# Kernel optimization log

Measured on AMD Instinct MI355X. Metric: run time of the kernel, lower is better.

## Reference

```python
import jax, jax.numpy as jnp
import numpy as np
from jax import lax

B, C, H, W = 32, 256, 64, 64
EPS = 1e-5


def setup_inputs() -> dict:
    key = jax.random.key(0)
    ks = jax.random.split(key, 4)
    x = jax.random.normal(ks[0], (B, C, H, W), dtype=jnp.float32)
    def mk(k):
        kw, = jax.random.split(k, 1)
        w = jax.random.normal(kw, (1, 2, 7, 7), dtype=jnp.float32) * 0.1  # OIHW
        gamma = jnp.ones((1,), jnp.float32)
        beta = jnp.zeros((1,), jnp.float32)
        rmean = jnp.zeros((1,), jnp.float32)
        rvar = jnp.ones((1,), jnp.float32)
        return w, gamma, beta, rmean, rvar
    w1, g1, b1, m1, v1 = mk(ks[1])
    w2, g2, b2, m2, v2 = mk(ks[2])
    w3, g3, b3, m3, v3 = mk(ks[3])
    return dict(x=x,
                w1=w1, g1=g1, b1=b1, m1=m1, v1=v1,
                w2=w2, g2=g2, b2=b2, m2=m2, v2=v2,
                w3=w3, g3=g3, b3=b3, m3=m3, v3=v3)


def _conv_bn_sig(p, w, gamma, beta, mean, var):
    # p: [B,2,h,w]; 7x7 conv 2->1, pad 3, no bias; BN (inference); sigmoid
    y = lax.conv_general_dilated(p, w, window_strides=(1, 1),
                                 padding=[(3, 3), (3, 3)],
                                 dimension_numbers=('NCHW', 'OIHW', 'NCHW'))
    r = lambda t: t.reshape(1, -1, 1, 1)
    y = (y - r(mean)) * (r(gamma) / jnp.sqrt(r(var) + EPS)) + r(beta)
    return jax.nn.sigmoid(y)


def reference(x, w1, g1, b1, m1, v1, w2, g2, b2, m2, v2, w3, g3, b3, m3, v3):
    # In this implementation the permutes cancel: all three branches pool over C.
    mx = jnp.max(x, axis=1, keepdims=True)
    av = jnp.mean(x, axis=1, keepdims=True)
    pooled = jnp.concatenate([mx, av], axis=1)              # [B,2,H,W]
    a1 = _conv_bn_sig(pooled, w1, g1, b1, m1, v1)           # [B,1,H,W]
    p2 = jnp.transpose(pooled, (0, 1, 3, 2))                # [B,2,W,H]
    a2 = jnp.transpose(_conv_bn_sig(p2, w2, g2, b2, m2, v2), (0, 1, 3, 2))
    a3 = _conv_bn_sig(pooled, w3, g3, b3, m3, v3)
    att = (a1 + a2 + a3) / 3.0
    return x * att
```

## Files before the change

### kernel.cpp

```cpp
#include <hip/hip_runtime.h>
#include <math.h>

#define NB 32
#define NC 256
#define NH 64
#define NW 64
#define NHW (NH * NW)
#define EPS_ 1e-5f

typedef float f32x4 __attribute__((ext_vector_type(4)));

__global__ __launch_bounds__(512) void pool_k(const float* __restrict__ x,
                                              float* __restrict__ pooled) {
    const int tid = threadIdx.x;
    const int chunk = tid >> 6;
    const int lane = tid & 63;
    const int q = blockIdx.x * 64 + lane;
    const int b = q >> 10;
    const int hwq = q & 1023;

    const float4* __restrict__ xq = (const float4*)x;
    const int base = b * NC * (NHW / 4) + hwq;

    float4 mx = make_float4(-INFINITY, -INFINITY, -INFINITY, -INFINITY);
    float4 sm = make_float4(0.f, 0.f, 0.f, 0.f);
    const int c0 = chunk * 32;
    #pragma unroll 8
    for (int c = c0; c < c0 + 32; ++c) {
        float4 v = xq[base + c * (NHW / 4)];
        mx.x = fmaxf(mx.x, v.x); mx.y = fmaxf(mx.y, v.y);
        mx.z = fmaxf(mx.z, v.z); mx.w = fmaxf(mx.w, v.w);
        sm.x += v.x; sm.y += v.y; sm.z += v.z; sm.w += v.w;
    }

    __shared__ float4 smax[8][64];
    __shared__ float4 ssum[8][64];
    smax[chunk][lane] = mx;
    ssum[chunk][lane] = sm;
    __syncthreads();

    if (tid < 64) {
        float4 m = smax[0][tid];
        float4 s = ssum[0][tid];
        #pragma unroll
        for (int k = 1; k < 8; ++k) {
            float4 m2 = smax[k][tid];
            float4 s2 = ssum[k][tid];
            m.x = fmaxf(m.x, m2.x); m.y = fmaxf(m.y, m2.y);
            m.z = fmaxf(m.z, m2.z); m.w = fmaxf(m.w, m2.w);
            s.x += s2.x; s.y += s2.y; s.z += s2.z; s.w += s2.w;
        }
        const float inv = 1.f / (float)NC;
        float4 mean = make_float4(s.x * inv, s.y * inv, s.z * inv, s.w * inv);
        float4* __restrict__ pq = (float4*)pooled;
        pq[(b * 2 + 0) * (NHW / 4) + hwq] = m;
        pq[(b * 2 + 1) * (NHW / 4) + hwq] = mean;
    }
}

__global__ __launch_bounds__(256) void att_k(
    const float* __restrict__ pooled,
    const float* __restrict__ w1, const float* __restrict__ g1,
    const float* __restrict__ be1, const float* __restrict__ m1,
    const float* __restrict__ v1,
    const float* __restrict__ w2, const float* __restrict__ g2,
    const float* __restrict__ be2, const float* __restrict__ m2,
    const float* __restrict__ v2,
    const float* __restrict__ w3, const float* __restrict__ g3,
    const float* __restrict__ be3, const float* __restrict__ m3,
    const float* __restrict__ v3,
    float* __restrict__ att) {
    const int gid = blockIdx.x * 256 + threadIdx.x;
    const int b = gid >> 12;
    const int hw = gid & (NHW - 1);
    const int h = hw >> 6;
    const int w = hw & 63;

    const float* __restrict__ pb = pooled + b * 2 * NHW;

    float s1 = 0.f, s2 = 0.f, s3 = 0.f;
    #pragma unroll
    for (int dh = -3; dh <= 3; ++dh) {
        const int y = h + dh;
        if ((unsigned)y >= (unsigned)NH) continue;
        #pragma unroll
        for (int dw = -3; dw <= 3; ++dw) {
            const int xx = w + dw;
            if ((unsigned)xx >= (unsigned)NW) continue;
            const int kh = dh + 3, kw = dw + 3;
            #pragma unroll
            for (int ci = 0; ci < 2; ++ci) {
                const float p = pb[ci * NHW + y * NW + xx];
                s1 = fmaf(p, w1[ci * 49 + kh * 7 + kw], s1);
                s2 = fmaf(p, w2[ci * 49 + kw * 7 + kh], s2);
                s3 = fmaf(p, w3[ci * 49 + kh * 7 + kw], s3);
            }
        }
    }

    const float sc1 = g1[0] * rsqrtf(v1[0] + EPS_);
    const float sc2 = g2[0] * rsqrtf(v2[0] + EPS_);
    const float sc3 = g3[0] * rsqrtf(v3[0] + EPS_);
    const float y1 = (s1 - m1[0]) * sc1 + be1[0];
    const float y2 = (s2 - m2[0]) * sc2 + be2[0];
    const float y3 = (s3 - m3[0]) * sc3 + be3[0];

    const float a1 = 1.f / (1.f + expf(-y1));
    const float a2 = 1.f / (1.f + expf(-y2));
    const float a3 = 1.f / (1.f + expf(-y3));

    att[gid] = (a1 + a2 + a3) * (1.f / 3.f);
}

__global__ __launch_bounds__(256) void mul_k(const float* __restrict__ x,
                                             const float* __restrict__ att,
                                             float* __restrict__ out) {
    const f32x4* __restrict__ xq = (const f32x4*)x;
    const f32x4* __restrict__ aq = (const f32x4*)att;
    f32x4* __restrict__ oq = (f32x4*)out;
    const int tid0 = blockIdx.x * 256 + threadIdx.x;
    #pragma unroll 4
    for (int it = 0; it < 16; ++it) {
        const int p = tid0 + it * 524288;
        const int b = p >> 18;
        const int hwq = p & 1023;
        const f32x4 a = aq[b * (NHW / 4) + hwq];
        const f32x4 v = xq[p];
        const f32x4 r = v * a;
        __builtin_nontemporal_store(r, &oq[p]);
    }
}

extern "C" void kernel_launch(void* const* d_in, const int* in_sizes, int n_in,
                              void* d_out, int out_size, void* d_ws, size_t ws_size,
                              hipStream_t stream) {
    const float* x  = (const float*)d_in[0];
    const float* w1 = (const float*)d_in[1];
    const float* g1 = (const float*)d_in[2];
    const float* b1 = (const float*)d_in[3];
    const float* m1 = (const float*)d_in[4];
    const float* v1 = (const float*)d_in[5];
    const float* w2 = (const float*)d_in[6];
    const float* g2 = (const float*)d_in[7];
    const float* b2 = (const float*)d_in[8];
    const float* m2 = (const float*)d_in[9];
    const float* v2 = (const float*)d_in[10];
    const float* w3 = (const float*)d_in[11];
    const float* g3 = (const float*)d_in[12];
    const float* b3 = (const float*)d_in[13];
    const float* m3 = (const float*)d_in[14];
    const float* v3 = (const float*)d_in[15];
    float* out = (float*)d_out;

    float* pooled = (float*)d_ws;
    float* att = (float*)((char*)d_ws + (size_t)NB * 2 * NHW * 4);

    pool_k<<<NB * NHW / 4 / 64, 512, 0, stream>>>(x, pooled);
    att_k<<<NB * NHW / 256, 256, 0, stream>>>(pooled,
        w1, g1, b1, m1, v1, w2, g2, b2, m2, v2, w3, g3, b3, m3, v3, att);
    mul_k<<<2048, 256, 0, stream>>>(x, att, out);
}
```

Before: 286.6 us.

## Fuse attention conv and broadcast multiply into one row-tiled kernel

Merges the attention-map convolution and the final x*att multiply into a single kernel where each block handles one (batch, row) pair. The block stages a padded 7-row halo of the pooled map in shared memory, computes 64 attention values with one wavefront, then all threads stream the 256 channels of that row. This removes a kernel launch and the global round trip of the attention map. In exchange, only 64 of 256 threads do the conv while the rest wait at a barrier. The multiply now reads short 256-byte row segments strided by channel rather than fully contiguous chunks.

```diff
diff --git a/kernel.cpp b/kernel.cpp
--- a/kernel.cpp
+++ b/kernel.cpp
@@ -58,7 +58,8 @@
     }
 }
 
-__global__ __launch_bounds__(256) void att_k(
+__global__ __launch_bounds__(256) void attmul_k(
+    const float* __restrict__ x,
     const float* __restrict__ pooled,
     const float* __restrict__ w1, const float* __restrict__ g1,
     const float* __restrict__ be1, const float* __restrict__ m1,
@@ -69,65 +70,73 @@
     const float* __restrict__ w3, const float* __restrict__ g3,
     const float* __restrict__ be3, const float* __restrict__ m3,
     const float* __restrict__ v3,
-    float* __restrict__ att) {
-    const int gid = blockIdx.x * 256 + threadIdx.x;
-    const int b = gid >> 12;
-    const int hw = gid & (NHW - 1);
-    const int h = hw >> 6;
-    const int w = hw & 63;
+    float* __restrict__ out) {
+    const int b = blockIdx.x >> 6;
+    const int h = blockIdx.x & 63;
+    const int t = threadIdx.x;
 
-    const float* __restrict__ pb = pooled + b * 2 * NHW;
+    __shared__ float plds[7][2][72];
+    __shared__ float att_s[64];
 
-    float s1 = 0.f, s2 = 0.f, s3 = 0.f;
     #pragma unroll
-    for (int dh = -3; dh <= 3; ++dh) {
-        const int y = h + dh;
-        if ((unsigned)y >= (unsigned)NH) continue;
+    for (int k = 0; k < 4; ++k) {
+        const int idx = t + k * 256;
+        if (idx < 1008) {
+            const int r = idx / 144;
+            const int rem = idx - r * 144;
+            const int ci = rem / 72;
+            const int col = rem - ci * 72;
+            const int y = h - 3 + r;
+            const int xcol = col - 3;
+            float v = 0.f;
+            if ((unsigned)y < (unsigned)NH && (unsigned)xcol < (unsigned)NW)
+                v = pooled[((b * 2 + ci) * NH + y) * NW + xcol];
+            plds[r][ci][col] = v;
+        }
+    }
+    __syncthreads();
+
+    if (t < 64) {
+        const int w = t;
+        float s1 = 0.f, s2 = 0.f, s3 = 0.f;
         #pragma unroll
-        for (int dw = -3; dw <= 3; ++dw) {
-            const int xx = w + dw;
-            if ((unsigned)xx >= (unsigned)NW) continue;
-            const int kh = dh + 3, kw = dw + 3;
+        for (int r = 0; r < 7; ++r) {
             #pragma unroll
             for (int ci = 0; ci < 2; ++ci) {
-                const float p = pb[ci * NHW + y * NW + xx];
-                s1 = fmaf(p, w1[ci * 49 + kh * 7 + kw], s1);
-                s2 = fmaf(p, w2[ci * 49 + kw * 7 + kh], s2);
-                s3 = fmaf(p, w3[ci * 49 + kh * 7 + kw], s3);
+                #pragma unroll
+                for (int dw = 0; dw < 7; ++dw) {
+                    const float p = plds[r][ci][w + dw];
+                    s1 = fmaf(p, w1[ci * 49 + r * 7 + dw], s1);
+                    s2 = fmaf(p, w2[ci * 49 + dw * 7 + r], s2);
+                    s3 = fmaf(p, w3[ci * 49 + r * 7 + dw], s3);
+                }
             }
         }
+        const float sc1 = g1[0] * rsqrtf(v1[0] + EPS_);
+        const float sc2 = g2[0] * rsqrtf(v2[0] + EPS_);
+        const float sc3 = g3[0] * rsqrtf(v3[0] + EPS_);
+        const float y1 = (s1 - m1[0]) * sc1 + be1[0];
+        const float y2 = (s2 - m2[0]) * sc2 + be2[0];
+        const float y3 = (s3 - m3[0]) * sc3 + be3[0];
+        const float a1 = 1.f / (1.f + expf(-y1));
+        const float a2 = 1.f / (1.f + expf(-y2));
+        const float a3 = 1.f / (1.f + expf(-y3));
+        att_s[w] = (a1 + a2 + a3) * (1.f / 3.f);
     }
+    __syncthreads();
 
-    const float sc1 = g1[0] * rsqrtf(v1[0] + EPS_);
-    const float sc2 = g2[0] * rsqrtf(v2[0] + EPS_);
-    const float sc3 = g3[0] * rsqrtf(v3[0] + EPS_);
-    const float y1 = (s1 - m1[0]) * sc1 + be1[0];
-    const float y2 = (s2 - m2[0]) * sc2 + be2[0];
-    const float y3 = (s3 - m3[0]) * sc3 + be3[0];
-
-    const float a1 = 1.f / (1.f + expf(-y1));
-    const float a2 = 1.f / (1.f + expf(-y2));
-    const float a3 = 1.f / (1.f + expf(-y3));
-
-    att[gid] = (a1 + a2 + a3) * (1.f / 3.f);
-}
-
-__global__ __launch_bounds__(256) void mul_k(const float* __restrict__ x,
-                                             const float* __restrict__ att,
-                                             float* __restrict__ out) {
     const f32x4* __restrict__ xq = (const f32x4*)x;
-    const f32x4* __restrict__ aq = (const f32x4*)att;
     f32x4* __restrict__ oq = (f32x4*)out;
-    const int tid0 = blockIdx.x * 256 + threadIdx.x;
+    const f32x4* __restrict__ a4 = (const f32x4*)att_s;
     #pragma unroll 4
-    for (int it = 0; it < 16; ++it) {
-        const int p = tid0 + it * 524288;
-        const int b = p >> 18;
-        const int hwq = p & 1023;
-        const f32x4 a = aq[b * (NHW / 4) + hwq];
-        const f32x4 v = xq[p];
-        const f32x4 r = v * a;
-        __builtin_nontemporal_store(r, &oq[p]);
+    for (int k = 0; k < 16; ++k) {
+        const int j = t + k * 256;
+        const int c = j >> 4;
+        const int wq = j & 15;
+        const int addr = (b * NC + c) * (NHW / 4) + h * 16 + wq;
+        const f32x4 v = xq[addr];
+        const f32x4 a = a4[wq];
+        __builtin_nontemporal_store(v * a, &oq[addr]);
     }
 }
 
@@ -153,10 +162,8 @@
     float* out = (float*)d_out;
 
     float* pooled = (float*)d_ws;
-    float* att = (float*)((char*)d_ws + (size_t)NB * 2 * NHW * 4);
 
     pool_k<<<NB * NHW / 4 / 64, 512, 0, stream>>>(x, pooled);
-    att_k<<<NB * NHW / 256, 256, 0, stream>>>(pooled,
-        w1, g1, b1, m1, v1, w2, g2, b2, m2, v2, w3, g3, b3, m3, v3, att);
-    mul_k<<<2048, 256, 0, stream>>>(x, att, out);
+    attmul_k<<<NB * NH, 256, 0, stream>>>(x, pooled,
+        w1, g1, b1, m1, v1, w2, g2, b2, m2, v2, w3, g3, b3, m3, v3, out);
 }
```

Measured after the change: 286.0 us. About the same (-0.2%).
